# Performance work log

Hardware: AMD Instinct MI355X
Metric: run time of the kernel (lower is better)

The kernel has to match this reference:

```python
import jax, jax.numpy as jnp
import numpy as np
import math

GAIN = 6.0
FREQ = 1000.0
Q = 0.707
SAMPLE_RATE = 44100


def _peaking_coeffs():
    # torchaudio.functional.equalizer_biquad coefficients (peaking EQ)
    w0 = 2.0 * math.pi * FREQ / SAMPLE_RATE
    A = math.exp(GAIN / 40.0 * math.log(10.0))
    alpha = math.sin(w0) / (2.0 * Q)
    b0 = 1.0 + alpha * A
    b1 = -2.0 * math.cos(w0)
    b2 = 1.0 - alpha * A
    a0 = 1.0 + alpha / A
    a1 = -2.0 * math.cos(w0)
    a2 = 1.0 - alpha / A
    # normalize by a0 (lfilter semantics)
    return (np.float32(b0 / a0), np.float32(b1 / a0), np.float32(b2 / a0),
            np.float32(a1 / a0), np.float32(a2 / a0))


def setup_inputs() -> dict:
    key = jax.random.key(0)
    x = jax.random.normal(key, (8, 2, 1200000), dtype=jnp.float32)
    return {"x": x}


def _biquad(x):
    # x: [B, C, T]; direct-form-I biquad with zero initial conditions
    b0, b1, b2, a1, a2 = _peaking_coeffs()
    # FIR part, fully vectorized: f[n] = b0*x[n] + b1*x[n-1] + b2*x[n-2]
    xp = jnp.pad(x, ((0, 0), (0, 0), (2, 0)))
    f = b0 * xp[..., 2:] + b1 * xp[..., 1:-1] + b2 * xp[..., :-2]
    # IIR part via scan over time: y[n] = f[n] - a1*y[n-1] - a2*y[n-2]
    f_t = jnp.moveaxis(f, -1, 0)  # [T, B, C]
    y0 = jnp.zeros(x.shape[:-1], dtype=x.dtype)

    def step(carry, ft):
        y1, y2 = carry
        y = ft - a1 * y1 - a2 * y2
        return (y, y1), y

    _, ys = jax.lax.scan(step, (y0, y0), f_t)
    return jnp.moveaxis(ys, 0, -1)  # [B, C, T]


def reference(x):
    return _biquad(x)
```

## Files before the change

kernel.cpp:

```cpp
#include <hip/hip_runtime.h>
#include <math.h>


typedef float f32x4 __attribute__((ext_vector_type(4)));

#define T_LEN 1200000
#define NCH   16
#define L     32
#define NR    64
#define NWARM 4
#define OUT_ROWS (NR - NWARM)
#define OUT_PER_SEG (OUT_ROWS * L)
#define SEGS_PER_CH (T_LEN / OUT_PER_SEG)
#define NSEG (SEGS_PER_CH * NCH)
#define WPB 4
#define NBLOCKS (NSEG / WPB)
#define RSTRIDE 36
#define WAVE_LDS (NR * RSTRIDE)

struct Params {
    float b0, b1, b2, a1, a2;
    float lnr, theta, inv_sinth;
    float C[3][4];
};

__global__ __launch_bounds__(256, 4) void eq_kernel(const float* __restrict__ x,
                                                    float* __restrict__ y, Params P)
{
    __shared__ __align__(16) float lds[WPB * WAVE_LDS];
    const int lane = threadIdx.x & 63;
    const int wid  = threadIdx.x >> 6;
    float* ys = lds + wid * WAVE_LDS;

    const int s  = blockIdx.x * WPB + wid;
    const int ch = s / SEGS_PER_CH;
    const int si = s - ch * SEGS_PER_CH;
    const float* __restrict__ xc = x + (size_t)ch * T_LEN;
    float*       __restrict__ yc = y + (size_t)ch * T_LEN;
    const int g0 = si * OUT_PER_SEG - NWARM * L;

    float c1r[4], c2r[4];
    {
        const int t0 = (lane << 2) & 31;
        float ph[5];
        #pragma unroll
        for (int k = 0; k < 5; ++k) {
            int t = t0 - 1 + k;
            ph[k] = (t < 0) ? 0.f
                            : expf(t * P.lnr) * sinf((t + 1) * P.theta) * P.inv_sinth;
        }
        #pragma unroll
        for (int k = 0; k < 4; ++k) {
            c1r[k] = fmaf(-P.a1, ph[k + 1], -P.a2 * ph[k]);
            c2r[k] = -P.a2 * ph[k + 1];
        }
    }

    f32x4 r[8];
    {
        const int gl = g0 + (lane << 5);
        #pragma unroll
        for (int k = 0; k < 8; ++k) {
            int g = gl + (k << 2);
            f32x4 v = {0.f, 0.f, 0.f, 0.f};
            if (g >= 0 && g < T_LEN) v = *(const f32x4*)(xc + g);
            r[k] = v;
        }
    }

    float x1 = __shfl_up(r[7].w, 1);
    float x2 = __shfl_up(r[7].z, 1);
    if (lane == 0) { x1 = 0.f; x2 = 0.f; }
    float v1 = 0.f, v2 = 0.f;
    const int base = lane * RSTRIDE;
    #pragma unroll
    for (int b = 0; b < 8; ++b) {
        f32x4 xv = r[b];
        f32x4 yv;
        #pragma unroll
        for (int k = 0; k < 4; ++k) {
            float xk = xv[k];
            float f  = fmaf(P.b0, xk, fmaf(P.b1, x1, P.b2 * x2));
            float t2 = fmaf(-P.a2, v2, f);
            float yk = fmaf(-P.a1, v1, t2);
            v2 = v1; v1 = yk;
            x2 = x1; x1 = xk;
            yv[k] = yk;
        }
        *(f32x4*)&ys[base + (b << 2)] = yv;
    }

    float q11 = __shfl_up(v1, 1), q21 = __shfl_up(v2, 1);
    float q12 = __shfl_up(v1, 2), q22 = __shfl_up(v2, 2);
    float q13 = __shfl_up(v1, 3), q23 = __shfl_up(v2, 3);
    float q14 = __shfl_up(v1, 4), q24 = __shfl_up(v2, 4);
    if (lane < 1) { q11 = 0.f; q21 = 0.f; }
    if (lane < 2) { q12 = 0.f; q22 = 0.f; }
    if (lane < 3) { q13 = 0.f; q23 = 0.f; }
    if (lane < 4) { q14 = 0.f; q24 = 0.f; }
    float e1 = q11, e2 = q21;
    e1 = fmaf(P.C[0][0], q12, fmaf(P.C[0][1], q22, e1));
    e2 = fmaf(P.C[0][2], q12, fmaf(P.C[0][3], q22, e2));
    e1 = fmaf(P.C[1][0], q13, fmaf(P.C[1][1], q23, e1));
    e2 = fmaf(P.C[1][2], q13, fmaf(P.C[1][3], q23, e2));
    e1 = fmaf(P.C[2][0], q14, fmaf(P.C[2][1], q24, e1));
    e2 = fmaf(P.C[2][2], q14, fmaf(P.C[2][3], q24, e2));

    const int j0 = (lane << 2) & 31;
    #pragma unroll
    for (int it = 0; it < 8; ++it) {
        int vo = (it << 6) + lane;
        int row = NWARM + (it << 3) + (lane >> 3);
        row = row > 63 ? 63 : row;
        float al = __shfl(e1, row);
        float be = __shfl(e2, row);
        if (vo < OUT_PER_SEG / 4) {
            f32x4 yv = *(const f32x4*)&ys[row * RSTRIDE + j0];
            f32x4 o;
            #pragma unroll
            for (int k = 0; k < 4; ++k)
                o[k] = fmaf(al, c1r[k], fmaf(be, c2r[k], yv[k]));
            int q = (vo << 2) + NWARM * L;
            *(f32x4*)(yc + g0 + q) = o;
        }
    }
}

extern "C" void kernel_launch(void* const* d_in, const int* in_sizes, int n_in,
                              void* d_out, int out_size, void* d_ws, size_t ws_size,
                              hipStream_t stream) {
    const float* x = (const float*)d_in[0];
    float* y = (float*)d_out;

    double w0    = 2.0 * M_PI * 1000.0 / 44100.0;
    double A     = exp(6.0 / 40.0 * log(10.0));
    double al    = sin(w0) / (2.0 * 0.707);
    double b0 = 1.0 + al * A;
    double b1 = -2.0 * cos(w0);
    double b2 = 1.0 - al * A;
    double a0 = 1.0 + al / A;
    double a1 = -2.0 * cos(w0);
    double a2 = 1.0 - al / A;
    b0 /= a0; b1 /= a0; b2 /= a0; a1 /= a0; a2 /= a0;

    Params P;
    P.b0 = (float)b0; P.b1 = (float)b1; P.b2 = (float)b2;
    P.a1 = (float)a1; P.a2 = (float)a2;

    double r     = sqrt(a2);
    double theta = acos(-a1 / (2.0 * r));
    P.lnr = (float)log(r);
    P.theta = (float)theta;
    P.inv_sinth = (float)(1.0 / sin(theta));

    double m00 = -a1, m01 = -a2, m10 = 1.0, m11 = 0.0;
    for (int s = 0; s < 5; ++s) {
        double t00 = m00 * m00 + m01 * m10;
        double t01 = m00 * m01 + m01 * m11;
        double t10 = m10 * m00 + m11 * m10;
        double t11 = m10 * m01 + m11 * m11;
        m00 = t00; m01 = t01; m10 = t10; m11 = t11;
    }
    double p00 = m00, p01 = m01, p10 = m10, p11 = m11;
    for (int k = 0; k < 3; ++k) {
        P.C[k][0] = (float)p00; P.C[k][1] = (float)p01;
        P.C[k][2] = (float)p10; P.C[k][3] = (float)p11;
        double t00 = p00 * m00 + p01 * m10;
        double t01 = p00 * m01 + p01 * m11;
        double t10 = p10 * m00 + p11 * m10;
        double t11 = p10 * m01 + p11 * m11;
        p00 = t00; p01 = t01; p10 = t10; p11 = t11;
    }

    eq_kernel<<<NBLOCKS, 256, 0, stream>>>(x, y, P);
}
```

Measured before the change: 30.74 us.

## Replace LDS correction pass with second register recurrence pass seeded by carry

Each lane now re-runs the biquad recurrence over its 32 samples, seeded with the corrected carry-in state, instead of staging zero-state outputs in LDS and adding an impulse-response correction. This removes the LDS buffer, the per-lane exp/sin coefficient setup and the shuffles used to broadcast corrections. Lanes then write their own 32 outputs directly with strided vector stores. The price is doubling the serial FMA chain per lane and giving up coalesced row stores; launch bounds are raised to allow more occupancy.

Result: slower. 47.20 us (+53.5%).

```diff
diff --git a/kernel.cpp b/kernel.cpp
--- a/kernel.cpp
+++ b/kernel.cpp
@@ -15,22 +15,17 @@
 #define NSEG (SEGS_PER_CH * NCH)
 #define WPB 4
 #define NBLOCKS (NSEG / WPB)
-#define RSTRIDE 36
-#define WAVE_LDS (NR * RSTRIDE)
 
 struct Params {
     float b0, b1, b2, a1, a2;
-    float lnr, theta, inv_sinth;
     float C[3][4];
 };
 
-__global__ __launch_bounds__(256, 4) void eq_kernel(const float* __restrict__ x,
+__global__ __launch_bounds__(256, 8) void eq_kernel(const float* __restrict__ x,
                                                     float* __restrict__ y, Params P)
 {
-    __shared__ __align__(16) float lds[WPB * WAVE_LDS];
     const int lane = threadIdx.x & 63;
     const int wid  = threadIdx.x >> 6;
-    float* ys = lds + wid * WAVE_LDS;
 
     const int s  = blockIdx.x * WPB + wid;
     const int ch = s / SEGS_PER_CH;
@@ -38,56 +33,36 @@
     const float* __restrict__ xc = x + (size_t)ch * T_LEN;
     float*       __restrict__ yc = y + (size_t)ch * T_LEN;
     const int g0 = si * OUT_PER_SEG - NWARM * L;
+    const int gl = g0 + (lane << 5);
 
-    float c1r[4], c2r[4];
-    {
-        const int t0 = (lane << 2) & 31;
-        float ph[5];
-        #pragma unroll
-        for (int k = 0; k < 5; ++k) {
-            int t = t0 - 1 + k;
-            ph[k] = (t < 0) ? 0.f
-                            : expf(t * P.lnr) * sinf((t + 1) * P.theta) * P.inv_sinth;
-        }
-        #pragma unroll
-        for (int k = 0; k < 4; ++k) {
-            c1r[k] = fmaf(-P.a1, ph[k + 1], -P.a2 * ph[k]);
-            c2r[k] = -P.a2 * ph[k + 1];
-        }
+    f32x4 r[8];
+    #pragma unroll
+    for (int k = 0; k < 8; ++k) {
+        int g = gl + (k << 2);
+        f32x4 v = {0.f, 0.f, 0.f, 0.f};
+        if (g >= 0 && g < T_LEN) v = *(const f32x4*)(xc + g);
+        r[k] = v;
     }
 
-    f32x4 r[8];
+    float tx1 = __shfl_up(r[7].w, 1);
+    float tx2 = __shfl_up(r[7].z, 1);
+    if (lane == 0) { tx1 = 0.f; tx2 = 0.f; }
+
+    float v1 = 0.f, v2 = 0.f;
     {
-        const int gl = g0 + (lane << 5);
+        float x1 = tx1, x2 = tx2;
         #pragma unroll
-        for (int k = 0; k < 8; ++k) {
-            int g = gl + (k << 2);
-            f32x4 v = {0.f, 0.f, 0.f, 0.f};
-            if (g >= 0 && g < T_LEN) v = *(const f32x4*)(xc + g);
-            r[k] = v;
+        for (int b = 0; b < 8; ++b) {
+            #pragma unroll
+            for (int k = 0; k < 4; ++k) {
+                float xk = r[b][k];
+                float f  = fmaf(P.b0, xk, fmaf(P.b1, x1, P.b2 * x2));
+                float t2 = fmaf(-P.a2, v2, f);
+                float yk = fmaf(-P.a1, v1, t2);
+                v2 = v1; v1 = yk;
+                x2 = x1; x1 = xk;
+            }
         }
-    }
-
-    float x1 = __shfl_up(r[7].w, 1);
-    float x2 = __shfl_up(r[7].z, 1);
-    if (lane == 0) { x1 = 0.f; x2 = 0.f; }
-    float v1 = 0.f, v2 = 0.f;
-    const int base = lane * RSTRIDE;
-    #pragma unroll
-    for (int b = 0; b < 8; ++b) {
-        f32x4 xv = r[b];
-        f32x4 yv;
-        #pragma unroll
-        for (int k = 0; k < 4; ++k) {
-            float xk = xv[k];
-            float f  = fmaf(P.b0, xk, fmaf(P.b1, x1, P.b2 * x2));
-            float t2 = fmaf(-P.a2, v2, f);
-            float yk = fmaf(-P.a1, v1, t2);
-            v2 = v1; v1 = yk;
-            x2 = x1; x1 = xk;
-            yv[k] = yk;
-        }
-        *(f32x4*)&ys[base + (b << 2)] = yv;
     }
 
     float q11 = __shfl_up(v1, 1), q21 = __shfl_up(v2, 1);
@@ -106,23 +81,30 @@
     e1 = fmaf(P.C[2][0], q14, fmaf(P.C[2][1], q24, e1));
     e2 = fmaf(P.C[2][2], q14, fmaf(P.C[2][3], q24, e2));
 
-    const int j0 = (lane << 2) & 31;
-    #pragma unroll
-    for (int it = 0; it < 8; ++it) {
-        int vo = (it << 6) + lane;
-        int row = NWARM + (it << 3) + (lane >> 3);
-        row = row > 63 ? 63 : row;
-        float al = __shfl(e1, row);
-        float be = __shfl(e2, row);
-        if (vo < OUT_PER_SEG / 4) {
-            f32x4 yv = *(const f32x4*)&ys[row * RSTRIDE + j0];
-            f32x4 o;
+    {
+        float x1 = tx1, x2 = tx2, w1 = e1, w2 = e2;
+        #pragma unroll
+        for (int b = 0; b < 8; ++b) {
+            f32x4 xv = r[b];
+            f32x4 yv;
             #pragma unroll
-            for (int k = 0; k < 4; ++k)
-                o[k] = fmaf(al, c1r[k], fmaf(be, c2r[k], yv[k]));
-            int q = (vo << 2) + NWARM * L;
-            *(f32x4*)(yc + g0 + q) = o;
+            for (int k = 0; k < 4; ++k) {
+                float xk = xv[k];
+                float f  = fmaf(P.b0, xk, fmaf(P.b1, x1, P.b2 * x2));
+                float t2 = fmaf(-P.a2, w2, f);
+                float yk = fmaf(-P.a1, w1, t2);
+                w2 = w1; w1 = yk;
+                x2 = x1; x1 = xk;
+                yv[k] = yk;
+            }
+            r[b] = yv;
         }
+    }
+
+    if (lane >= NWARM) {
+        #pragma unroll
+        for (int k = 0; k < 8; ++k)
+            *(f32x4*)(yc + gl + (k << 2)) = r[k];
     }
 }
 
@@ -147,12 +129,6 @@
     P.b0 = (float)b0; P.b1 = (float)b1; P.b2 = (float)b2;
     P.a1 = (float)a1; P.a2 = (float)a2;
 
-    double r     = sqrt(a2);
-    double theta = acos(-a1 / (2.0 * r));
-    P.lnr = (float)log(r);
-    P.theta = (float)theta;
-    P.inv_sinth = (float)(1.0 / sin(theta));
-
     double m00 = -a1, m01 = -a2, m10 = 1.0, m11 = 0.0;
     for (int s = 0; s < 5; ++s) {
         double t00 = m00 * m00 + m01 * m10;
```
